# Performance work log

Measured on AMD Instinct MI355X. Metric: run time of the kernel, lower is better.

The kernel has to match this reference:

```python
import jax, jax.numpy as jnp
import numpy as np

B, V = 4, 10242
N = B * V            # 40968 packed vertices
E_PER = 30720        # edges per mesh
HID = 128


def _bilinear_sample(fm, grid):
    """pytorch3d vert_align core: grid_sample(align_corners=True, bilinear).
    fm: [B,C,H,W], grid: [B,V,2] xy in [-1,1] -> [B,V,C]."""
    b_, c_, h_, w_ = fm.shape
    x = (grid[..., 0] + 1.0) * 0.5 * (w_ - 1)
    y = (grid[..., 1] + 1.0) * 0.5 * (h_ - 1)
    x0f, y0f = jnp.floor(x), jnp.floor(y)
    wx1, wy1 = x - x0f, y - y0f
    wx0, wy0 = 1.0 - wx1, 1.0 - wy1
    x0 = jnp.clip(x0f, 0, w_ - 1).astype(jnp.int32)
    x1 = jnp.clip(x0f + 1, 0, w_ - 1).astype(jnp.int32)
    y0 = jnp.clip(y0f, 0, h_ - 1).astype(jnp.int32)
    y1 = jnp.clip(y0f + 1, 0, h_ - 1).astype(jnp.int32)
    fmt = jnp.transpose(fm, (0, 2, 3, 1))  # [B,H,W,C]
    bi = jnp.arange(b_)[:, None]
    g = lambda yy, xx: fmt[bi, yy, xx]     # [B,V,C]
    return ((wy0 * wx0)[..., None] * g(y0, x0)
            + (wy0 * wx1)[..., None] * g(y0, x1)
            + (wy1 * wx0)[..., None] * g(y1, x0)
            + (wy1 * wx1)[..., None] * g(y1, x1))


def _graph_conv(x, edges, w0, b0, w1, b1):
    """pytorch3d GraphConv (undirected): W0 x_i + sum over both edge dirs of W1 x_j."""
    h0 = x @ w0 + b0
    h1 = x @ w1 + b1
    e0, e1 = edges[:, 0], edges[:, 1]
    agg = jnp.zeros_like(h0).at[e0].add(h1[e1]).at[e1].add(h1[e0])
    return h0 + agg


def setup_inputs() -> dict:
    key = jax.random.key(0)
    ks = jax.random.split(key, 20)
    s = 0.05
    # per-mesh edges, offset into packed index space
    e = jax.random.randint(ks[0], (B, E_PER, 2), 0, V)
    e = e + (jnp.arange(B) * V)[:, None, None]
    return {
        "feat1": jax.random.normal(ks[1], (B, 256, 56, 56), jnp.float32),
        "feat2": jax.random.normal(ks[2], (B, 512, 28, 28), jnp.float32),
        "feat3": jax.random.normal(ks[3], (B, 1024, 14, 14), jnp.float32),
        "feat4": jax.random.normal(ks[4], (B, 2048, 7, 7), jnp.float32),
        "aligned_verts": jax.random.uniform(ks[5], (B, V, 3), jnp.float32, -1.0, 1.0),
        "verts_packed": jax.random.normal(ks[6], (N, 3), jnp.float32),
        "image_enc": jax.random.normal(ks[7], (B, 256), jnp.float32),
        "edges": e.reshape(B * E_PER, 2).astype(jnp.int64),
        "bottleneck_w": jax.random.normal(ks[8], (3840, HID), jnp.float32) * s,
        "bottleneck_b": jnp.zeros((HID,), jnp.float32),
        "g0_w0": jax.random.normal(ks[9], (387, HID), jnp.float32) * s,
        "g0_b0": jnp.zeros((HID,), jnp.float32),
        "g0_w1": jax.random.normal(ks[10], (387, HID), jnp.float32) * s,
        "g0_b1": jnp.zeros((HID,), jnp.float32),
        "gw0": jax.random.normal(ks[11], (7, HID, HID), jnp.float32) * s,
        "gb0": jnp.zeros((7, HID), jnp.float32),
        "gw1": jax.random.normal(ks[12], (7, HID, HID), jnp.float32) * s,
        "gb1": jnp.zeros((7, HID), jnp.float32),
        "off_w": jax.random.normal(ks[13], (HID, 3), jnp.float32) * s,
        "off_b": jnp.zeros((3,), jnp.float32),
    }


def reference(feat1, feat2, feat3, feat4, aligned_verts, verts_packed, image_enc,
              edges, bottleneck_w, bottleneck_b, g0_w0, g0_b0, g0_w1, g0_b1,
              gw0, gb0, gw1, gb1, off_w, off_b):
    grid = aligned_verts[..., :2]  # vert_align uses xy only
    samp = jnp.concatenate([_bilinear_sample(f, grid)
                            for f in (feat1, feat2, feat3, feat4)], axis=-1)
    samp = samp.reshape(N, 3840)  # return_packed=True
    vfeat = jax.nn.relu(samp @ bottleneck_w + bottleneck_b)
    enc = jnp.repeat(image_enc, V, axis=0)  # repeat_interleave
    x = jnp.concatenate([vfeat, verts_packed, enc], axis=1)  # [N,387]
    x = jax.nn.relu(_graph_conv(x, edges, g0_w0, g0_b0, g0_w1, g0_b1))
    for i in range(7):
        x = jax.nn.relu(_graph_conv(x, edges, gw0[i], gb0[i], gw1[i], gb1[i]))
    return x @ off_w + off_b  # delta_v [N,3]
```

## Files before the change

kernel.cpp:

```cpp
#include <hip/hip_runtime.h>

static inline int ceil_div(int a, int b) { return (a + b - 1) / b; }

typedef __attribute__((ext_vector_type(8))) short short8;
typedef __attribute__((ext_vector_type(4))) float floatx4;

__device__ __forceinline__ unsigned short f2bf(float f) {
    unsigned int u = __float_as_uint(f);
    unsigned int r = (u + 0x7fffu + ((u >> 16) & 1u)) >> 16;
    return (unsigned short)r;
}
__device__ __forceinline__ float bf2f(unsigned short h) {
    return __uint_as_float(((unsigned int)h) << 16);
}

__global__ __launch_bounds__(1024) void scan1_k(const int* __restrict__ deg,
                                                int* __restrict__ excl,
                                                int* __restrict__ bsum, int Nv) {
    __shared__ int s[1024];
    int tid = threadIdx.x;
    int i = blockIdx.x * 1024 + tid;
    int v = (i < Nv) ? deg[i] : 0;
    s[tid] = v;
    __syncthreads();
    for (int off = 1; off < 1024; off <<= 1) {
        int t = (tid >= off) ? s[tid - off] : 0;
        __syncthreads();
        if (tid >= off) s[tid] += t;
        __syncthreads();
    }
    if (i < Nv) excl[i] = s[tid] - v;
    if (tid == 1023) bsum[blockIdx.x] = s[1023];
}

__global__ __launch_bounds__(64) void scan2_k(int* __restrict__ bsum, int nb) {
    __shared__ int s[64];
    int tid = threadIdx.x;
    int v = (tid < nb) ? bsum[tid] : 0;
    s[tid] = v;
    __syncthreads();
    for (int off = 1; off < 64; off <<= 1) {
        int t = (tid >= off) ? s[tid - off] : 0;
        __syncthreads();
        if (tid >= off) s[tid] += t;
        __syncthreads();
    }
    if (tid < nb) bsum[tid] = s[tid] - v;
}

__global__ __launch_bounds__(1024) void scan3_k(const int* __restrict__ excl,
                                                const int* __restrict__ bsum,
                                                const int* __restrict__ deg,
                                                int* __restrict__ rowptr,
                                                int* __restrict__ cursor, int Nv) {
    int i = blockIdx.x * 1024 + threadIdx.x;
    if (i < Nv) {
        int val = excl[i] + bsum[blockIdx.x];
        rowptr[i] = val;
        cursor[i] = val;
        if (i == Nv - 1) rowptr[Nv] = val + deg[i];
    }
}

__global__ __launch_bounds__(256) void fill_adj_k(const int* __restrict__ edges,
                                                  int* __restrict__ cursor,
                                                  int* __restrict__ adj, int E) {
    int e = blockIdx.x * blockDim.x + threadIdx.x;
    if (e < E) {
        int a = edges[2 * e], b = edges[2 * e + 1];
        adj[atomicAdd(&cursor[a], 1)] = b;
        adj[atomicAdd(&cursor[b], 1)] = a;
    }
}

__global__ __launch_bounds__(256) void fatpre_k(const int* __restrict__ edges,
                                                int* __restrict__ deg, int E, int nE,
                                                const float* __restrict__ g0w0,
                                                const float* __restrict__ g0w1,
                                                const float* __restrict__ gw0,
                                                const float* __restrict__ gw1,
                                                unsigned short* __restrict__ Wt,
                                                const float* __restrict__ bw,
                                                unsigned short* __restrict__ bwT,
                                                const float* __restrict__ enc,
                                                float* __restrict__ encp, int B_) {
    int bid = blockIdx.x;
    int tid = threadIdx.x;
    if (bid < nE) {
        int e = bid * 256 + tid;
        if (e < E) {
            atomicAdd(&deg[edges[2 * e]], 1);
            atomicAdd(&deg[edges[2 * e + 1]], 1);
        }
    } else if (bid < nE + 16) {
        int lh = bid - nE;
        int l = lh >> 1, h = lh & 1;
        const float* src;
        if (l == 0) src = h ? g0w1 : g0w0;
        else src = (h ? gw1 : gw0) + (size_t)(l - 1) * 16384;
        unsigned short* dst = Wt + (size_t)lh * 16384;
        for (int idx = tid; idx < 16384; idx += 256) {
            int n = idx >> 7, k = idx & 127;
            dst[n * 128 + k] = f2bf(src[k * 128 + n]);
        }
    } else if (bid < nE + 46) {
        int blk = bid - nE - 16;
        for (int idx = tid; idx < 16384; idx += 256) {
            int n = idx >> 7, kk = idx & 127;
            bwT[(size_t)n * 3840 + blk * 128 + kk] =
                f2bf(bw[(size_t)(blk * 128 + kk) * 128 + n]);
        }
    } else {
        int b = bid - nE - 46;
        int sH = tid >> 7;
        int j = tid & 127;
        const float* w = sH ? g0w1 : g0w0;
        const float* eb = enc + b * 256;
        float acc = 0.f;
        for (int c = 0; c < 256; ++c) acc = fmaf(eb[c], w[(131 + c) * 128 + j], acc);
        encp[(sH * B_ + b) * 128 + j] = acc;
    }
}

__global__ __launch_bounds__(256) void proj_all_k(
    const float* __restrict__ fm1, const float* __restrict__ fm2,
    const float* __restrict__ fm3, const float* __restrict__ fm4,
    const unsigned short* __restrict__ bwT, float* __restrict__ q1, float* __restrict__ q2,
    float* __restrict__ q3, float* __restrict__ q4, int B_) {
    __shared__ unsigned short wlds[8192];

    int tid = threadIdx.x;
    int n1 = 49 * B_ * 4, n2 = 13 * B_ * 8, n3 = 4 * B_ * 16;
    int bid = blockIdx.x;
    const float* fm;
    float* op;
    int C, HW, PT, idx, koff;
    if (bid < n1) {
        fm = fm1; op = q1; C = 256; HW = 3136; PT = 49; idx = bid; koff = 0;
    } else if (bid < n1 + n2) {
        fm = fm2; op = q2; C = 512; HW = 784; PT = 13; idx = bid - n1; koff = 256;
    } else if (bid < n1 + n2 + n3) {
        fm = fm3; op = q3; C = 1024; HW = 196; PT = 4; idx = bid - n1 - n2; koff = 768;
    } else {
        fm = fm4; op = q4; C = 2048; HW = 49; PT = 1; idx = bid - n1 - n2 - n3; koff = 1792;
    }
    int pt = idx % PT;
    int r2 = idx / PT;
    int b = r2 % B_;
    int zz = r2 / B_;
    int p0 = pt * 64;
    int S = B_ * HW * 128;
    const float* fmb = fm + (size_t)b * C * HW;
    int kcf = zz * 64;
    int kcw = koff + kcf;

#pragma unroll
    for (int l = 0; l < 4; ++l) {
        int i2 = tid + l * 256;
        int n = i2 >> 3, c16 = i2 & 7;
        *(short8*)&wlds[n * 64 + ((c16 ^ (n & 7)) * 8)] =
            *(const short8*)(bwT + (size_t)n * 3840 + kcw + c16 * 8);
    }

    int wave = tid >> 6, lane = tid & 63;
    int row16 = lane & 15, quad = lane >> 4;
    int p = p0 + wave * 16 + row16;
    bool pok = (p < HW);
    int pc = pok ? p : 0;
    short8 ax[2];
#pragma unroll
    for (int ks = 0; ks < 2; ++ks) {
#pragma unroll
        for (int j = 0; j < 8; ++j) {
            float v = pok ? fmb[(size_t)(kcf + ks * 32 + quad * 8 + j) * HW + pc] : 0.f;
            ax[ks][j] = (short)f2bf(v);
        }
    }
    __syncthreads();

    floatx4 acc[8];
#pragma unroll
    for (int j = 0; j < 8; ++j) acc[j] = (floatx4){0.f, 0.f, 0.f, 0.f};
#pragma unroll
    for (int ks = 0; ks < 2; ++ks) {
        int c = ks * 4 + quad;
#pragma unroll
        for (int nt = 0; nt < 8; ++nt) {
            int wr = nt * 16 + row16;
            short8 bwf = *(short8*)&wlds[wr * 64 + ((c ^ (wr & 7)) * 8)];
            acc[nt] = __builtin_amdgcn_mfma_f32_16x16x32_bf16(ax[ks], bwf, acc[nt], 0, 0, 0);
        }
    }

    float* obase = op + (size_t)zz * S + (size_t)b * HW * 128;
#pragma unroll
    for (int nt = 0; nt < 8; ++nt) {
        int colg = nt * 16 + row16;
#pragma unroll
        for (int rr = 0; rr < 4; ++rr) {
            int pr = p0 + wave * 16 + quad * 4 + rr;
            if (pr < HW) obase[(size_t)pr * 128 + colg] = acc[nt][rr];
        }
    }
}

__global__ __launch_bounds__(256) void reduce4_k(const float* __restrict__ q1,
                                                 const float* __restrict__ q2,
                                                 const float* __restrict__ q3,
                                                 const float* __restrict__ q4,
                                                 float* __restrict__ o1, float* __restrict__ o2,
                                                 float* __restrict__ o3, float* __restrict__ o4,
                                                 int S1, int S2, int S3, int S4) {
    int i = (blockIdx.x * 256 + threadIdx.x) * 4;
    const float* src;
    float* dst;
    int S, z, base;
    if (i < S1) {
        src = q1; dst = o1; S = S1; z = 4; base = i;
    } else if (i < S1 + S2) {
        src = q2; dst = o2; S = S2; z = 8; base = i - S1;
    } else if (i < S1 + S2 + S3) {
        src = q3; dst = o3; S = S3; z = 16; base = i - S1 - S2;
    } else if (i < S1 + S2 + S3 + S4) {
        src = q4; dst = o4; S = S4; z = 32; base = i - S1 - S2 - S3;
    } else {
        return;
    }
    float4 a = *(const float4*)(src + base);
    for (int zz = 1; zz < z; ++zz) {
        float4 b = *(const float4*)(src + (size_t)zz * S + base);
        a.x += b.x; a.y += b.y; a.z += b.z; a.w += b.w;
    }
    *(float4*)(dst + base) = a;
}

__device__ __forceinline__ float sample_level(const float* __restrict__ pp, int Hh, int Ww,
                                              float gx, float gy, int j) {
    float x = (gx + 1.f) * 0.5f * (float)(Ww - 1);
    float y = (gy + 1.f) * 0.5f * (float)(Hh - 1);
    float x0f = floorf(x), y0f = floorf(y);
    float wx1 = x - x0f, wy1 = y - y0f;
    float wx0 = 1.f - wx1, wy0 = 1.f - wy1;
    int x0 = (int)fminf(fmaxf(x0f, 0.f), (float)(Ww - 1));
    int x1 = (int)fminf(fmaxf(x0f + 1.f, 0.f), (float)(Ww - 1));
    int y0 = (int)fminf(fmaxf(y0f, 0.f), (float)(Hh - 1));
    int y1 = (int)fminf(fmaxf(y0f + 1.f, 0.f), (float)(Hh - 1));
    const float* r00 = pp + (size_t)(y0 * Ww + x0) * 128;
    const float* r01 = pp + (size_t)(y0 * Ww + x1) * 128;
    const float* r10 = pp + (size_t)(y1 * Ww + x0) * 128;
    const float* r11 = pp + (size_t)(y1 * Ww + x1) * 128;
    return wy0 * (wx0 * r00[j] + wx1 * r01[j]) + wy1 * (wx0 * r10[j] + wx1 * r11[j]);
}

__global__ __launch_bounds__(128) void sample_bottleneck_k(
    const float* __restrict__ av, const float* __restrict__ pp1, const float* __restrict__ pp2,
    const float* __restrict__ pp3, const float* __restrict__ pp4, const float* __restrict__ bb,
    const float* __restrict__ verts, const float* __restrict__ encp,
    const float* __restrict__ g0w0, const float* __restrict__ g0w1,
    const float* __restrict__ g0b0, const float* __restrict__ g0b1,
    unsigned short* __restrict__ X, unsigned short* __restrict__ H, int V_, int B_) {
    int n = blockIdx.x, j = threadIdx.x;
    int b = n / V_;
    float gx = av[(size_t)n * 3 + 0];
    float gy = av[(size_t)n * 3 + 1];
    float acc = bb[j];
    acc += sample_level(pp1 + (size_t)b * 3136 * 128, 56, 56, gx, gy, j);
    acc += sample_level(pp2 + (size_t)b * 784 * 128, 28, 28, gx, gy, j);
    acc += sample_level(pp3 + (size_t)b * 196 * 128, 14, 14, gx, gy, j);
    acc += sample_level(pp4 + (size_t)b * 49 * 128, 7, 7, gx, gy, j);
    X[(size_t)n * 128 + j] = f2bf(fmaxf(acc, 0.f));
    float v0 = verts[n * 3 + 0], v1 = verts[n * 3 + 1], v2 = verts[n * 3 + 2];
    float h0 = encp[(0 * B_ + b) * 128 + j] + g0b0[j] + v0 * g0w0[128 * 128 + j] +
               v1 * g0w0[129 * 128 + j] + v2 * g0w0[130 * 128 + j];
    float h1 = encp[(1 * B_ + b) * 128 + j] + g0b1[j] + v0 * g0w1[128 * 128 + j] +
               v1 * g0w1[129 * 128 + j] + v2 * g0w1[130 * 128 + j];
    H[(size_t)n * 256 + j] = f2bf(h0);
    H[(size_t)n * 256 + 128 + j] = f2bf(h1);
}


__global__ __launch_bounds__(256) void aggpre_k(const unsigned short* __restrict__ H,
                                                const int* __restrict__ rowptr,
                                                const int* __restrict__ adj,
                                                float* __restrict__ pre, int Nv) {
    int wave = threadIdx.x >> 6, lane = threadIdx.x & 63;
    int n0 = (blockIdx.x * 4 + wave) * 2;
    if (n0 >= Nv) return;
    int r0 = rowptr[n0], r1 = rowptr[n0 + 1], r2 = rowptr[n0 + 2];
    unsigned int u0 = *(const unsigned int*)(H + (size_t)n0 * 256 + 2 * lane);
    unsigned int u1 = *(const unsigned int*)(H + (size_t)(n0 + 1) * 256 + 2 * lane);
    float a0 = bf2f((unsigned short)(u0 & 0xffff));
    float a1 = bf2f((unsigned short)(u0 >> 16));
    float b0 = bf2f((unsigned short)(u1 & 0xffff));
    float b1 = bf2f((unsigned short)(u1 >> 16));
    int tA = r0, tB = r1;
    while (tA < r1 || tB < r2) {
        int nbA[8], nbB[8];
        unsigned int wA[8], wB[8];
#pragma unroll
        for (int q = 0; q < 8; ++q) {
            int ia = tA + q; ia = (ia < r1) ? ia : (r1 - 1); ia = (ia < 0) ? 0 : ia;
            nbA[q] = adj[ia];
            int ib = tB + q; ib = (ib < r2) ? ib : (r2 - 1); ib = (ib < 0) ? 0 : ib;
            nbB[q] = adj[ib];
        }
#pragma unroll
        for (int q = 0; q < 8; ++q) {
            wA[q] = *(const unsigned int*)(H + (size_t)nbA[q] * 256 + 128 + 2 * lane);
            wB[q] = *(const unsigned int*)(H + (size_t)nbB[q] * 256 + 128 + 2 * lane);
        }
#pragma unroll
        for (int q = 0; q < 8; ++q) {
            if (tA + q < r1) {
                a0 += bf2f((unsigned short)(wA[q] & 0xffff));
                a1 += bf2f((unsigned short)(wA[q] >> 16));
            }
            if (tB + q < r2) {
                b0 += bf2f((unsigned short)(wB[q] & 0xffff));
                b1 += bf2f((unsigned short)(wB[q] >> 16));
            }
        }
        tA += 8;
        tB += 8;
    }
    pre[(size_t)n0 * 128 + 2 * lane] = a0;
    pre[(size_t)n0 * 128 + 2 * lane + 1] = a1;
    pre[(size_t)(n0 + 1) * 128 + 2 * lane] = b0;
    pre[(size_t)(n0 + 1) * 128 + 2 * lane + 1] = b1;
}

__global__ __launch_bounds__(256) void agg_x_k(const unsigned short* __restrict__ X,
                                               const int* __restrict__ rowptr,
                                               const int* __restrict__ adj,
                                               unsigned short* __restrict__ Agg, int Nv) {
    int wave = threadIdx.x >> 6, lane = threadIdx.x & 63;
    int n0 = (blockIdx.x * 4 + wave) * 2;
    if (n0 >= Nv) return;
    const unsigned int* Xu = (const unsigned int*)X;
    int r0 = rowptr[n0], r1 = rowptr[n0 + 1], r2 = rowptr[n0 + 2];
    float a0 = 0.f, a1 = 0.f, b0 = 0.f, b1 = 0.f;
    int tA = r0, tB = r1;
    while (tA < r1 || tB < r2) {
        int nbA[8], nbB[8];
        unsigned int wA[8], wB[8];
#pragma unroll
        for (int q = 0; q < 8; ++q) {
            int ia = tA + q; ia = (ia < r1) ? ia : (r1 - 1); ia = (ia < 0) ? 0 : ia;
            nbA[q] = adj[ia];
            int ib = tB + q; ib = (ib < r2) ? ib : (r2 - 1); ib = (ib < 0) ? 0 : ib;
            nbB[q] = adj[ib];
        }
#pragma unroll
        for (int q = 0; q < 8; ++q) {
            wA[q] = Xu[(size_t)nbA[q] * 64 + lane];
            wB[q] = Xu[(size_t)nbB[q] * 64 + lane];
        }
#pragma unroll
        for (int q = 0; q < 8; ++q) {
            if (tA + q < r1) {
                a0 += bf2f((unsigned short)(wA[q] & 0xffff));
                a1 += bf2f((unsigned short)(wA[q] >> 16));
            }
            if (tB + q < r2) {
                b0 += bf2f((unsigned short)(wB[q] & 0xffff));
                b1 += bf2f((unsigned short)(wB[q] >> 16));
            }
        }
        tA += 8;
        tB += 8;
    }
    unsigned int oA = (unsigned int)f2bf(a0) | ((unsigned int)f2bf(a1) << 16);
    unsigned int oB = (unsigned int)f2bf(b0) | ((unsigned int)f2bf(b1) << 16);
    *(unsigned int*)(Agg + (size_t)n0 * 128 + 2 * lane) = oA;
    *(unsigned int*)(Agg + (size_t)(n0 + 1) * 128 + 2 * lane) = oB;
}

__global__ __launch_bounds__(256, 3) void gemm_dual_k(
    const unsigned short* __restrict__ Xin, const unsigned short* __restrict__ Agg,
    const unsigned short* __restrict__ Wt,
    const float* __restrict__ b0, const float* __restrict__ b1,
    const float* __restrict__ pre, const int* __restrict__ degv,
    unsigned short* __restrict__ Xout, int M) {
    __shared__ unsigned short wlds[16384];
    __shared__ unsigned short cs[64 * 72];
    __shared__ float bS[128];

    int tid = threadIdx.x;
    int m0 = blockIdx.x * 128;
    int yb = blockIdx.y;

    int wave = tid >> 6, lane = tid & 63;
    int row16 = lane & 15;
    int quad = lane >> 4;
    int wrow = wave * 16;

    short8 axT[2][4], agT[2][4];
    int dgT[2][4];
    {
        int g = min(m0 + wrow + row16, M - 1);
#pragma unroll
        for (int ks = 0; ks < 4; ++ks) {
            int koff = ks * 32 + quad * 8;
            axT[0][ks] = *(const short8*)(Xin + (size_t)g * 128 + koff);
            agT[0][ks] = *(const short8*)(Agg + (size_t)g * 128 + koff);
        }
#pragma unroll
        for (int rr = 0; rr < 4; ++rr)
            dgT[0][rr] = degv[min(m0 + wrow + quad * 4 + rr, M - 1)];
    }

    if (tid < 64) {
        bS[tid] = b0 ? b0[yb * 64 + tid] : 0.f;
        bS[64 + tid] = b1 ? b1[yb * 64 + tid] : 0.f;
    }

    const unsigned short* W0h = Wt + (size_t)yb * 64 * 128;
    const unsigned short* W1h = Wt + 16384 + (size_t)yb * 64 * 128;
#pragma unroll
    for (int l = 0; l < 8; ++l) {
        int idx = tid + l * 256;
        int half = idx >> 10;
        int r = (idx >> 4) & 63;
        int c16 = idx & 15;
        int sw = (c16 ^ (r & 15)) * 8;
        const unsigned short* src = (half ? W1h : W0h) + r * 128 + c16 * 8;
        *(short8*)&wlds[half * 8192 + r * 128 + sw] = *(const short8*)src;
    }
    __syncthreads();

    {
        int g = min(m0 + 64 + wrow + row16, M - 1);
#pragma unroll
        for (int ks = 0; ks < 4; ++ks) {
            int koff = ks * 32 + quad * 8;
            axT[1][ks] = *(const short8*)(Xin + (size_t)g * 128 + koff);
            agT[1][ks] = *(const short8*)(Agg + (size_t)g * 128 + koff);
        }
#pragma unroll
        for (int rr = 0; rr < 4; ++rr)
            dgT[1][rr] = degv[min(m0 + 64 + wrow + quad * 4 + rr, M - 1)];
    }

#pragma unroll
    for (int t = 0; t < 2; ++t) {
        int mT = m0 + t * 64;
        floatx4 acc[4];
#pragma unroll
        for (int j = 0; j < 4; j++) acc[j] = (floatx4){0.f, 0.f, 0.f, 0.f};

#pragma unroll
        for (int ks = 0; ks < 4; ++ks) {
            int c = ks * 4 + quad;
#pragma unroll
            for (int nt = 0; nt < 4; ++nt) {
                int wr = nt * 16 + row16;
                short8 bw0 = *(short8*)&wlds[wr * 128 + ((c ^ row16) * 8)];
                short8 bw1 = *(short8*)&wlds[8192 + wr * 128 + ((c ^ row16) * 8)];
                acc[nt] = __builtin_amdgcn_mfma_f32_16x16x32_bf16(axT[t][ks], bw0, acc[nt], 0, 0, 0);
                acc[nt] = __builtin_amdgcn_mfma_f32_16x16x32_bf16(agT[t][ks], bw1, acc[nt], 0, 0, 0);
            }
        }

#pragma unroll
        for (int nt = 0; nt < 4; ++nt) {
            int colh = nt * 16 + row16;
            int colg = yb * 64 + colh;
            float bc0 = bS[colh];
            float bc1 = bS[64 + colh];
#pragma unroll
            for (int rr = 0; rr < 4; ++rr) {
                int row = wrow + quad * 4 + rr;
                int gm = mT + row;
                float v = acc[nt][rr] + bc0 + (float)dgT[t][rr] * bc1;
                if (pre && gm < M) v += pre[(size_t)gm * 128 + colg];
                cs[row * 72 + colh] = f2bf(fmaxf(v, 0.f));
            }
        }
        __syncthreads();

        {
            int r = tid >> 2;
            int cq = (tid & 3) * 16;
            int gm = mT + r;
            if (gm < M) {
                unsigned short* dst = Xout + (size_t)gm * 128 + yb * 64 + cq;
                *(short8*)dst = *(short8*)&cs[r * 72 + cq];
                *(short8*)(dst + 8) = *(short8*)&cs[r * 72 + cq + 8];
            }
        }
        __syncthreads();
    }
}

__global__ __launch_bounds__(256) void head_k(const unsigned short* __restrict__ X,
                                              const float* __restrict__ off_w,
                                              const float* __restrict__ off_b,
                                              float* __restrict__ out, int Nv) {
    int wave = threadIdx.x >> 6, lane = threadIdx.x & 63;
    int n = blockIdx.x * 4 + wave;
    if (n >= Nv) return;
    unsigned int u = *(const unsigned int*)(X + (size_t)n * 128 + 2 * lane);
    float x0 = bf2f((unsigned short)(u & 0xffff));
    float x1 = bf2f((unsigned short)(u >> 16));
    int c0 = 2 * lane, c1 = 2 * lane + 1;
    float p0 = x0 * off_w[c0 * 3 + 0] + x1 * off_w[c1 * 3 + 0];
    float p1 = x0 * off_w[c0 * 3 + 1] + x1 * off_w[c1 * 3 + 1];
    float p2 = x0 * off_w[c0 * 3 + 2] + x1 * off_w[c1 * 3 + 2];
#pragma unroll
    for (int m = 1; m < 64; m <<= 1) {
        p0 += __shfl_xor(p0, m);
        p1 += __shfl_xor(p1, m);
        p2 += __shfl_xor(p2, m);
    }
    if (lane == 0) {
        out[n * 3 + 0] = p0 + off_b[0];
        out[n * 3 + 1] = p1 + off_b[1];
        out[n * 3 + 2] = p2 + off_b[2];
    }
}

extern "C" void kernel_launch(void* const* d_in, const int* in_sizes, int n_in, void* d_out,
                              int out_size, void* d_ws, size_t ws_size, hipStream_t stream) {
    const float* feat1 = (const float*)d_in[0];
    const float* feat2 = (const float*)d_in[1];
    const float* feat3 = (const float*)d_in[2];
    const float* feat4 = (const float*)d_in[3];
    const float* av = (const float*)d_in[4];
    const float* verts = (const float*)d_in[5];
    const float* image_enc = (const float*)d_in[6];
    const int* edges = (const int*)d_in[7];
    const float* bw = (const float*)d_in[8];
    const float* bb = (const float*)d_in[9];
    const float* g0w0 = (const float*)d_in[10];
    const float* g0b0 = (const float*)d_in[11];
    const float* g0w1 = (const float*)d_in[12];
    const float* g0b1 = (const float*)d_in[13];
    const float* gw0 = (const float*)d_in[14];
    const float* gb0 = (const float*)d_in[15];
    const float* gw1 = (const float*)d_in[16];
    const float* gb1 = (const float*)d_in[17];
    const float* off_w = (const float*)d_in[18];
    const float* off_b = (const float*)d_in[19];

    int B_ = in_sizes[6] / 256;
    int N_ = in_sizes[5] / 3;
    int V_ = N_ / B_;
    int E_ = in_sizes[7] / 2;

    char* wsb = (char*)d_ws;
    size_t off = 0;
    auto alloc = [&](size_t bytes) -> void* {
        void* p = (void*)(wsb + off);
        off += (bytes + 255) & ~(size_t)255;
        return p;
    };
    int S1 = B_ * 3136 * 128;
    int S2 = B_ * 784 * 128;
    int S3 = B_ * 196 * 128;
    int S4 = B_ * 49 * 128;
    float* pp1 = (float*)alloc((size_t)S1 * 4);
    float* pp2 = (float*)alloc((size_t)S2 * 4);
    float* pp3 = (float*)alloc((size_t)S3 * 4);
    float* pp4 = (float*)alloc((size_t)S4 * 4);
    float* q1 = (float*)alloc((size_t)4 * S1 * 4);
    float* q2 = (float*)alloc((size_t)8 * S2 * 4);
    float* q3 = (float*)alloc((size_t)16 * S3 * 4);
    float* q4 = (float*)alloc((size_t)32 * S4 * 4);
    unsigned short* XA = (unsigned short*)alloc((size_t)N_ * 128 * 2);
    unsigned short* XB = (unsigned short*)alloc((size_t)N_ * 128 * 2);
    unsigned short* AggB = (unsigned short*)alloc((size_t)N_ * 128 * 2);
    unsigned short* Hb = (unsigned short*)alloc((size_t)N_ * 256 * 2);
    float* pre = (float*)alloc((size_t)N_ * 128 * 4);
    unsigned short* Wt = (unsigned short*)alloc((size_t)8 * 2 * 128 * 128 * 2);
    unsigned short* bwT = (unsigned short*)alloc((size_t)128 * 3840 * 2);
    float* encp = (float*)alloc((size_t)2 * B_ * 128 * 4);
    int* deg = (int*)alloc((size_t)(N_ + 1) * 4);
    int* rowptr = (int*)alloc((size_t)(N_ + 1) * 4);
    int* cursor = (int*)alloc((size_t)N_ * 4);
    int* excl = (int*)alloc((size_t)N_ * 4);
    int* bsum = (int*)alloc((size_t)64 * 4);
    int* adj = (int*)alloc((size_t)2 * E_ * 4);

    hipMemsetAsync(deg, 0, (N_ + 1) * sizeof(int), stream);

    int nE = ceil_div(E_, 256);
    fatpre_k<<<nE + 46 + B_, 256, 0, stream>>>(edges, deg, E_, nE, g0w0, g0w1, gw0, gw1, Wt,
                                               bw, bwT, image_enc, encp, B_);

    int nb = ceil_div(N_, 1024);
    scan1_k<<<nb, 1024, 0, stream>>>(deg, excl, bsum, N_);
    scan2_k<<<1, 64, 0, stream>>>(bsum, nb);
    scan3_k<<<nb, 1024, 0, stream>>>(excl, bsum, deg, rowptr, cursor, N_);
    fill_adj_k<<<ceil_div(E_, 256), 256, 0, stream>>>(edges, cursor, adj, E_);

    int nproj = 49 * B_ * 4 + 13 * B_ * 8 + 4 * B_ * 16 + 1 * B_ * 32;
    proj_all_k<<<nproj, 256, 0, stream>>>(feat1, feat2, feat3, feat4, bwT, q1, q2, q3, q4, B_);
    int tot4 = (S1 + S2 + S3 + S4) / 4;
    reduce4_k<<<ceil_div(tot4, 256), 256, 0, stream>>>(q1, q2, q3, q4, pp1, pp2, pp3, pp4, S1,
                                                       S2, S3, S4);

    sample_bottleneck_k<<<N_, 128, 0, stream>>>(av, pp1, pp2, pp3, pp4, bb, verts, encp, g0w0,
                                                g0w1, g0b0, g0b1, XA, Hb, V_, B_);

    int agrid = ceil_div(N_, 8);

    aggpre_k<<<agrid, 256, 0, stream>>>(Hb, rowptr, adj, pre, N_);

    dim3 ggrid(ceil_div(N_, 128), 2);
    agg_x_k<<<agrid, 256, 0, stream>>>(XA, rowptr, adj, AggB, N_);
    gemm_dual_k<<<ggrid, 256, 0, stream>>>(XA, AggB, Wt, nullptr, nullptr, pre, deg, XB, N_);
    unsigned short* Xc = XB;
    unsigned short* Xn = XA;
    for (int i = 0; i < 7; ++i) {
        agg_x_k<<<agrid, 256, 0, stream>>>(Xc, rowptr, adj, AggB, N_);
        gemm_dual_k<<<ggrid, 256, 0, stream>>>(Xc, AggB, Wt + (size_t)(i + 1) * 32768,
                                               gb0 + i * 128, gb1 + i * 128, nullptr, deg, Xn,
                                               N_);
        unsigned short* t = Xc;
        Xc = Xn;
        Xn = t;
    }
    head_k<<<ceil_div(N_, 4), 256, 0, stream>>>(Xc, off_w, off_b, (float*)d_out, N_);
}
```

Baseline: 472.6 us.

## Replace split-K partial buffers with atomics and fuse layer-0 aggregations

The projection kernel now accumulates its split-K partial products directly into the zero-initialised pyramid buffers with float atomicAdd, so the large partial buffers and the separate reduce kernel go away. The two layer-0 neighbour aggregations (over X and over the H half) are merged into one kernel that writes both sums as bf16, and the GEMM epilogue adds H0 and the aggregated H directly instead of reading an fp32 pre buffer. This saves a launch and a lot of intermediate traffic, at the cost of atomic contention, a memset, nondeterministic summation order, and extra bf16 rounding of the aggregated H term.

```diff
diff --git a/kernel.cpp b/kernel.cpp
--- a/kernel.cpp
+++ b/kernel.cpp
@@ -125,8 +125,8 @@
 __global__ __launch_bounds__(256) void proj_all_k(
     const float* __restrict__ fm1, const float* __restrict__ fm2,
     const float* __restrict__ fm3, const float* __restrict__ fm4,
-    const unsigned short* __restrict__ bwT, float* __restrict__ q1, float* __restrict__ q2,
-    float* __restrict__ q3, float* __restrict__ q4, int B_) {
+    const unsigned short* __restrict__ bwT, float* __restrict__ o1, float* __restrict__ o2,
+    float* __restrict__ o3, float* __restrict__ o4, int B_) {
     __shared__ unsigned short wlds[8192];
 
     int tid = threadIdx.x;
@@ -136,20 +136,19 @@
     float* op;
     int C, HW, PT, idx, koff;
     if (bid < n1) {
-        fm = fm1; op = q1; C = 256; HW = 3136; PT = 49; idx = bid; koff = 0;
+        fm = fm1; op = o1; C = 256; HW = 3136; PT = 49; idx = bid; koff = 0;
     } else if (bid < n1 + n2) {
-        fm = fm2; op = q2; C = 512; HW = 784; PT = 13; idx = bid - n1; koff = 256;
+        fm = fm2; op = o2; C = 512; HW = 784; PT = 13; idx = bid - n1; koff = 256;
     } else if (bid < n1 + n2 + n3) {
-        fm = fm3; op = q3; C = 1024; HW = 196; PT = 4; idx = bid - n1 - n2; koff = 768;
+        fm = fm3; op = o3; C = 1024; HW = 196; PT = 4; idx = bid - n1 - n2; koff = 768;
     } else {
-        fm = fm4; op = q4; C = 2048; HW = 49; PT = 1; idx = bid - n1 - n2 - n3; koff = 1792;
+        fm = fm4; op = o4; C = 2048; HW = 49; PT = 1; idx = bid - n1 - n2 - n3; koff = 1792;
     }
     int pt = idx % PT;
     int r2 = idx / PT;
     int b = r2 % B_;
     int zz = r2 / B_;
     int p0 = pt * 64;
-    int S = B_ * HW * 128;
     const float* fmb = fm + (size_t)b * C * HW;
     int kcf = zz * 64;
     int kcw = koff + kcf;
@@ -192,46 +191,16 @@
         }
     }
 
-    float* obase = op + (size_t)zz * S + (size_t)b * HW * 128;
+    float* obase = op + (size_t)b * HW * 128;
 #pragma unroll
     for (int nt = 0; nt < 8; ++nt) {
         int colg = nt * 16 + row16;
 #pragma unroll
         for (int rr = 0; rr < 4; ++rr) {
             int pr = p0 + wave * 16 + quad * 4 + rr;
-            if (pr < HW) obase[(size_t)pr * 128 + colg] = acc[nt][rr];
-        }
-    }
-}
-
-__global__ __launch_bounds__(256) void reduce4_k(const float* __restrict__ q1,
-                                                 const float* __restrict__ q2,
-                                                 const float* __restrict__ q3,
-                                                 const float* __restrict__ q4,
-                                                 float* __restrict__ o1, float* __restrict__ o2,
-                                                 float* __restrict__ o3, float* __restrict__ o4,
-                                                 int S1, int S2, int S3, int S4) {
-    int i = (blockIdx.x * 256 + threadIdx.x) * 4;
-    const float* src;
-    float* dst;
-    int S, z, base;
-    if (i < S1) {
-        src = q1; dst = o1; S = S1; z = 4; base = i;
-    } else if (i < S1 + S2) {
-        src = q2; dst = o2; S = S2; z = 8; base = i - S1;
-    } else if (i < S1 + S2 + S3) {
-        src = q3; dst = o3; S = S3; z = 16; base = i - S1 - S2;
-    } else if (i < S1 + S2 + S3 + S4) {
-        src = q4; dst = o4; S = S4; z = 32; base = i - S1 - S2 - S3;
-    } else {
-        return;
-    }
-    float4 a = *(const float4*)(src + base);
-    for (int zz = 1; zz < z; ++zz) {
-        float4 b = *(const float4*)(src + (size_t)zz * S + base);
-        a.x += b.x; a.y += b.y; a.z += b.z; a.w += b.w;
-    }
-    *(float4*)(dst + base) = a;
+            if (pr < HW) atomicAdd(&obase[(size_t)pr * 128 + colg], acc[nt][rr]);
+        }
+    }
 }
 
 __device__ __forceinline__ float sample_level(const float* __restrict__ pp, int Hh, int Ww,
@@ -278,25 +247,23 @@
     H[(size_t)n * 256 + 128 + j] = f2bf(h1);
 }
 
-
-__global__ __launch_bounds__(256) void aggpre_k(const unsigned short* __restrict__ H,
-                                                const int* __restrict__ rowptr,
-                                                const int* __restrict__ adj,
-                                                float* __restrict__ pre, int Nv) {
+__global__ __launch_bounds__(256) void agg0_k(const unsigned short* __restrict__ X,
+                                              const unsigned short* __restrict__ H,
+                                              const int* __restrict__ rowptr,
+                                              const int* __restrict__ adj,
+                                              unsigned short* __restrict__ AggX,
+                                              unsigned short* __restrict__ AggH, int Nv) {
     int wave = threadIdx.x >> 6, lane = threadIdx.x & 63;
     int n0 = (blockIdx.x * 4 + wave) * 2;
     if (n0 >= Nv) return;
+    const unsigned int* Xu = (const unsigned int*)X;
     int r0 = rowptr[n0], r1 = rowptr[n0 + 1], r2 = rowptr[n0 + 2];
-    unsigned int u0 = *(const unsigned int*)(H + (size_t)n0 * 256 + 2 * lane);
-    unsigned int u1 = *(const unsigned int*)(H + (size_t)(n0 + 1) * 256 + 2 * lane);
-    float a0 = bf2f((unsigned short)(u0 & 0xffff));
-    float a1 = bf2f((unsigned short)(u0 >> 16));
-    float b0 = bf2f((unsigned short)(u1 & 0xffff));
-    float b1 = bf2f((unsigned short)(u1 >> 16));
+    float a0 = 0.f, a1 = 0.f, b0 = 0.f, b1 = 0.f;
+    float c0 = 0.f, c1 = 0.f, d0 = 0.f, d1 = 0.f;
     int tA = r0, tB = r1;
     while (tA < r1 || tB < r2) {
         int nbA[8], nbB[8];
-        unsigned int wA[8], wB[8];
+        unsigned int wA[8], wB[8], hA[8], hB[8];
 #pragma unroll
         for (int q = 0; q < 8; ++q) {
             int ia = tA + q; ia = (ia < r1) ? ia : (r1 - 1); ia = (ia < 0) ? 0 : ia;
@@ -306,27 +273,37 @@
         }
 #pragma unroll
         for (int q = 0; q < 8; ++q) {
-            wA[q] = *(const unsigned int*)(H + (size_t)nbA[q] * 256 + 128 + 2 * lane);
-            wB[q] = *(const unsigned int*)(H + (size_t)nbB[q] * 256 + 128 + 2 * lane);
+            wA[q] = Xu[(size_t)nbA[q] * 64 + lane];
+            wB[q] = Xu[(size_t)nbB[q] * 64 + lane];
+            hA[q] = *(const unsigned int*)(H + (size_t)nbA[q] * 256 + 128 + 2 * lane);
+            hB[q] = *(const unsigned int*)(H + (size_t)nbB[q] * 256 + 128 + 2 * lane);
         }
 #pragma unroll
         for (int q = 0; q < 8; ++q) {
             if (tA + q < r1) {
                 a0 += bf2f((unsigned short)(wA[q] & 0xffff));
                 a1 += bf2f((unsigned short)(wA[q] >> 16));
+                c0 += bf2f((unsigned short)(hA[q] & 0xffff));
+                c1 += bf2f((unsigned short)(hA[q] >> 16));
             }
             if (tB + q < r2) {
                 b0 += bf2f((unsigned short)(wB[q] & 0xffff));
                 b1 += bf2f((unsigned short)(wB[q] >> 16));
+                d0 += bf2f((unsigned short)(hB[q] & 0xffff));
+                d1 += bf2f((unsigned short)(hB[q] >> 16));
             }
         }
         tA += 8;
         tB += 8;
     }
-    pre[(size_t)n0 * 128 + 2 * lane] = a0;
-    pre[(size_t)n0 * 128 + 2 * lane + 1] = a1;
-    pre[(size_t)(n0 + 1) * 128 + 2 * lane] = b0;
-    pre[(size_t)(n0 + 1) * 128 + 2 * lane + 1] = b1;
+    *(unsigned int*)(AggX + (size_t)n0 * 128 + 2 * lane) =
+        (unsigned int)f2bf(a0) | ((unsigned int)f2bf(a1) << 16);
+    *(unsigned int*)(AggX + (size_t)(n0 + 1) * 128 + 2 * lane) =
+        (unsigned int)f2bf(b0) | ((unsigned int)f2bf(b1) << 16);
+    *(unsigned int*)(AggH + (size_t)n0 * 128 + 2 * lane) =
+        (unsigned int)f2bf(c0) | ((unsigned int)f2bf(c1) << 16);
+    *(unsigned int*)(AggH + (size_t)(n0 + 1) * 128 + 2 * lane) =
+        (unsigned int)f2bf(d0) | ((unsigned int)f2bf(d1) << 16);
 }
 
 __global__ __launch_bounds__(256) void agg_x_k(const unsigned short* __restrict__ X,
@@ -379,8 +356,8 @@
     const unsigned short* __restrict__ Xin, const unsigned short* __restrict__ Agg,
     const unsigned short* __restrict__ Wt,
     const float* __restrict__ b0, const float* __restrict__ b1,
-    const float* __restrict__ pre, const int* __restrict__ degv,
-    unsigned short* __restrict__ Xout, int M) {
+    const unsigned short* __restrict__ h0b, const unsigned short* __restrict__ aggh,
+    const int* __restrict__ degv, unsigned short* __restrict__ Xout, int M) {
     __shared__ unsigned short wlds[16384];
     __shared__ unsigned short cs[64 * 72];
     __shared__ float bS[128];
@@ -472,7 +449,9 @@
                 int row = wrow + quad * 4 + rr;
                 int gm = mT + row;
                 float v = acc[nt][rr] + bc0 + (float)dgT[t][rr] * bc1;
-                if (pre && gm < M) v += pre[(size_t)gm * 128 + colg];
+                if (h0b && gm < M)
+                    v += bf2f(h0b[(size_t)gm * 256 + colg]) +
+                         bf2f(aggh[(size_t)gm * 128 + colg]);
                 cs[row * 72 + colh] = f2bf(fmaxf(v, 0.f));
             }
         }
@@ -562,15 +541,12 @@
     float* pp2 = (float*)alloc((size_t)S2 * 4);
     float* pp3 = (float*)alloc((size_t)S3 * 4);
     float* pp4 = (float*)alloc((size_t)S4 * 4);
-    float* q1 = (float*)alloc((size_t)4 * S1 * 4);
-    float* q2 = (float*)alloc((size_t)8 * S2 * 4);
-    float* q3 = (float*)alloc((size_t)16 * S3 * 4);
-    float* q4 = (float*)alloc((size_t)32 * S4 * 4);
+    size_t pp_bytes = off;
     unsigned short* XA = (unsigned short*)alloc((size_t)N_ * 128 * 2);
     unsigned short* XB = (unsigned short*)alloc((size_t)N_ * 128 * 2);
     unsigned short* AggB = (unsigned short*)alloc((size_t)N_ * 128 * 2);
+    unsigned short* AggH = (unsigned short*)alloc((size_t)N_ * 128 * 2);
     unsigned short* Hb = (unsigned short*)alloc((size_t)N_ * 256 * 2);
-    float* pre = (float*)alloc((size_t)N_ * 128 * 4);
     unsigned short* Wt = (unsigned short*)alloc((size_t)8 * 2 * 128 * 128 * 2);
     unsigned short* bwT = (unsigned short*)alloc((size_t)128 * 3840 * 2);
     float* encp = (float*)alloc((size_t)2 * B_ * 128 * 4);
@@ -582,6 +558,7 @@
     int* adj = (int*)alloc((size_t)2 * E_ * 4);
 
     hipMemsetAsync(deg, 0, (N_ + 1) * sizeof(int), stream);
+    hipMemsetAsync(wsb, 0, pp_bytes, stream);
 
     int nE = ceil_div(E_, 256);
     fatpre_k<<<nE + 46 + B_, 256, 0, stream>>>(edges, deg, E_, nE, g0w0, g0w1, gw0, gw1, Wt,
@@ -594,28 +571,25 @@
     fill_adj_k<<<ceil_div(E_, 256), 256, 0, stream>>>(edges, cursor, adj, E_);
 
     int nproj = 49 * B_ * 4 + 13 * B_ * 8 + 4 * B_ * 16 + 1 * B_ * 32;
-    proj_all_k<<<nproj, 256, 0, stream>>>(feat1, feat2, feat3, feat4, bwT, q1, q2, q3, q4, B_);
-    int tot4 = (S1 + S2 + S3 + S4) / 4;
-    reduce4_k<<<ceil_div(tot4, 256), 256, 0, stream>>>(q1, q2, q3, q4, pp1, pp2, pp3, pp4, S1,
-                                                       S2, S3, S4);
+    proj_all_k<<<nproj, 256, 0, stream>>>(feat1, feat2, feat3, feat4, bwT, pp1, pp2, pp3, pp4,
+                                          B_);
 
     sample_bottleneck_k<<<N_, 128, 0, stream>>>(av, pp1, pp2, pp3, pp4, bb, verts, encp, g0w0,
                                                 g0w1, g0b0, g0b1, XA, Hb, V_, B_);
 
     int agrid = ceil_div(N_, 8);
 
-    aggpre_k<<<agrid, 256, 0, stream>>>(Hb, rowptr, adj, pre, N_);
-
     dim3 ggrid(ceil_div(N_, 128), 2);
-    agg_x_k<<<agrid, 256, 0, stream>>>(XA, rowptr, adj, AggB, N_);
-    gemm_dual_k<<<ggrid, 256, 0, stream>>>(XA, AggB, Wt, nullptr, nullptr, pre, deg, XB, N_);
+    agg0_k<<<agrid, 256, 0, stream>>>(XA, Hb, rowptr, adj, AggB, AggH, N_);
+    gemm_dual_k<<<ggrid, 256, 0, stream>>>(XA, AggB, Wt, nullptr, nullptr, Hb, AggH, deg, XB,
+                                           N_);
     unsigned short* Xc = XB;
     unsigned short* Xn = XA;
     for (int i = 0; i < 7; ++i) {
         agg_x_k<<<agrid, 256, 0, stream>>>(Xc, rowptr, adj, AggB, N_);
         gemm_dual_k<<<ggrid, 256, 0, stream>>>(Xc, AggB, Wt + (size_t)(i + 1) * 32768,
-                                               gb0 + i * 128, gb1 + i * 128, nullptr, deg, Xn,
-                                               N_);
+                                               gb0 + i * 128, gb1 + i * 128, nullptr, nullptr,
+                                               deg, Xn, N_);
         unsigned short* t = Xc;
         Xc = Xn;
         Xn = t;
```

New measurement: 471.5 us. Within noise of the previous version (-0.2%).
